# Kernel optimization log

Hardware: AMD Instinct MI355X
Metric: run time of the kernel (lower is better)

The kernel has to match this reference:

```python
import jax, jax.numpy as jnp
import numpy as np

N = 50000      # nodes
E = 800000     # edges
SEQ, SS = 96, 32
D = 128        # node feat dim = seqdim + ssdim
HE = 32        # edge hidden dim
HEADS = 4
DEPTH = 8
EPS = 1e-5
SLOPE = 0.01   # torch default leaky_relu slope (used in DGL EGATConv and LayerBlock)


def setup_inputs() -> dict:
    key = jax.random.key(0)
    ks = jax.random.split(key, 24)
    rn = lambda k, s: jax.random.normal(k, s, jnp.float32) * 0.1
    return {
        'sequence': jax.random.randint(ks[0], (N,), 0, 21),
        'secondary': jax.random.randint(ks[1], (N,), 0, 3),
        'edge_p': jax.random.uniform(ks[2], (E,), jnp.float32),
        'src': jax.random.randint(ks[3], (E,), 0, N),
        'dst': jax.random.randint(ks[4], (E,), 0, N),
        'Wseq': rn(ks[5], (21, SEQ)),
        'Wsec': rn(ks[6], (3, SS)),
        'W0_node': rn(ks[7], (D, D)), 'b0_node': jnp.zeros((D,), jnp.float32),
        'W0_ni': rn(ks[8], (D, HE)), 'W0_fij': rn(ks[9], (1, HE)),
        'W0_nj': rn(ks[10], (D, HE)), 'attn0': rn(ks[11], (1, HE)),
        'ebias0': jnp.zeros((HE,), jnp.float32),
        'Wn': rn(ks[12], (DEPTH, D, D)), 'bn': jnp.zeros((DEPTH, D), jnp.float32),
        'Wni': rn(ks[13], (DEPTH, D, HE)), 'Wfij': rn(ks[14], (DEPTH, HE, HE)),
        'Wnj': rn(ks[15], (DEPTH, D, HE)), 'attnB': rn(ks[16], (DEPTH, HEADS, HE // HEADS)),
        'ebiasB': jnp.zeros((DEPTH, HE), jnp.float32),
        'gn': jnp.ones((DEPTH, D), jnp.float32), 'betan': jnp.zeros((DEPTH, D), jnp.float32),
        'ge': jnp.ones((DEPTH, HE), jnp.float32), 'betae': jnp.zeros((DEPTH, HE), jnp.float32),
        'Wfc': rn(ks[17], (D, 1)), 'bfc': jnp.zeros((1,), jnp.float32),
    }


def _edge_softmax(logits, dst):
    # softmax over incoming edges of each destination node; logits: (E, H)
    m = jax.ops.segment_max(logits, dst, num_segments=N)
    m = jnp.where(jnp.isfinite(m), m, 0.0)
    z = jnp.exp(logits - m[dst])
    s = jax.ops.segment_sum(z, dst, num_segments=N)
    return z / s[dst]


def _egat(h, e, src, dst, Wnode, bnode, Wni_, Wfij_, Wnj_, attn, ebias, heads):
    # DGL EGATConv: h (N, Din), e (E, De) -> h_out (N, H, on), f_out (E, H, oe)
    oe = Wni_.shape[1] // heads
    on = Wnode.shape[1] // heads
    f = h[src] @ Wni_ + e @ Wfij_ + h[dst] @ Wnj_ + ebias          # (E, H*oe)
    f = jax.nn.leaky_relu(f, SLOPE).reshape(E, heads, oe)
    logits = jnp.einsum('ehd,hd->eh', f, attn)                      # (E, H)
    a = _edge_softmax(logits, dst)                                  # (E, H)
    hp = (h @ Wnode + bnode).reshape(N, heads, on)
    h_out = jax.ops.segment_sum(hp[src] * a[..., None], dst, num_segments=N)
    return h_out, f


def _batchnorm(x, gamma, beta):
    mu = x.mean(0)
    var = x.var(0)  # biased, as torch BN training mode
    return (x - mu) * jax.lax.rsqrt(var + EPS) * gamma + beta


def reference(sequence, secondary, edge_p, src, dst, Wseq, Wsec,
              W0_node, b0_node, W0_ni, W0_fij, W0_nj, attn0, ebias0,
              Wn, bn, Wni, Wfij, Wnj, attnB, ebiasB,
              gn, betan, ge, betae, Wfc, bfc):
    h = jnp.concatenate([Wseq[sequence], Wsec[secondary]], axis=1)   # (N, D)
    e = edge_p[:, None]                                              # (E, 1)
    h, f = _egat(h, e, src, dst, W0_node, b0_node, W0_ni, W0_fij, W0_nj, attn0, ebias0, 1)
    h = h.reshape(N, D)
    e = f.reshape(E, HE)

    def block(carry, p):
        hh, ee = carry
        Wn_, bn_, Wni_, Wfij_, Wnj_, attn_, eb_, gn_, btn_, ge_, bte_ = p
        h2, f2 = _egat(hh, ee, src, dst, Wn_, bn_, Wni_, Wfij_, Wnj_, attn_, eb_, HEADS)
        h2 = jax.nn.leaky_relu(_batchnorm(h2.reshape(N, D), gn_, btn_), SLOPE)
        e2 = jax.nn.leaky_relu(_batchnorm(f2.reshape(E, HE), ge_, bte_), SLOPE)
        return (h2, e2), None

    (h, e), _ = jax.lax.scan(block, (h, e),
                             (Wn, bn, Wni, Wfij, Wnj, attnB, ebiasB, gn, betan, ge, betae))
    return h @ Wfc + bfc                                             # (N, 1)
```

## Files before the change

### kernel.cpp

```cpp
#include <hip/hip_runtime.h>

#define NN 50000
#define NE 800000
#define D 128
#define HE 32
#define HEADS 4
#define DEPTH 8
#define EPSV 1e-5f
#define SLOPE 0.01f
#define CHUNK 196
#define SBH 512
#define SBE 1024

__device__ __forceinline__ float lrelu(float x) { return x > 0.f ? x : SLOPE * x; }

__device__ __forceinline__ float bf2f(unsigned short u) {
    union { float f; unsigned i; } c;
    c.i = ((unsigned)u) << 16;
    return c.f;
}
__device__ __forceinline__ unsigned short f2bf(float f) {
    union { float f; unsigned i; } c;
    c.f = f;
    unsigned r = c.i + 0x7FFFu + ((c.i >> 16) & 1u);
    return (unsigned short)(r >> 16);
}
__device__ __forceinline__ unsigned pack2(float a, float b) {
    return (unsigned)f2bf(a) | ((unsigned)f2bf(b) << 16);
}
__device__ __forceinline__ void unpk2(unsigned u, float& a, float& b) {
    union { float f; unsigned i; } c;
    c.i = u << 16; a = c.f;
    c.i = u & 0xFFFF0000u; b = c.f;
}

__global__ void k_init_h(const int* __restrict__ seq, const int* __restrict__ sec,
                         const float* __restrict__ Wseq, const float* __restrict__ Wsec,
                         float* __restrict__ h) {
    int n = blockIdx.x;
    int d = threadIdx.x;
    float v = (d < 96) ? Wseq[seq[n] * 96 + d] : Wsec[sec[n] * 32 + (d - 96)];
    h[(size_t)n * D + d] = v;
}

__global__ void k_count(const int* __restrict__ dst, int* __restrict__ cnt) {
    int e = blockIdx.x * blockDim.x + threadIdx.x;
    if (e < NE) atomicAdd(&cnt[dst[e]], 1);
}

__global__ void k_bsum(const int* __restrict__ cnt, int* __restrict__ bsum) {
    __shared__ int sh[256];
    int b = blockIdx.x, tid = threadIdx.x;
    int idx = b * CHUNK + tid;
    int v = (tid < CHUNK && idx < NN) ? cnt[idx] : 0;
    sh[tid] = v;
    __syncthreads();
    for (int st = 128; st >= 1; st >>= 1) {
        if (tid < st) sh[tid] += sh[tid + st];
        __syncthreads();
    }
    if (tid == 0) bsum[b] = sh[0];
}

__global__ void k_bscan(const int* __restrict__ bsum, int* __restrict__ bscan,
                        int* __restrict__ indptr) {
    __shared__ int sh[256];
    int tid = threadIdx.x;
    int v = bsum[tid];
    sh[tid] = v;
    __syncthreads();
    for (int st = 1; st < 256; st <<= 1) {
        int t = (tid >= st) ? sh[tid - st] : 0;
        __syncthreads();
        sh[tid] += t;
        __syncthreads();
    }
    bscan[tid] = sh[tid] - v;
    if (tid == 255) indptr[NN] = sh[255];
}

__global__ void k_bwrite(const int* __restrict__ cnt, const int* __restrict__ bscan,
                         int* __restrict__ indptr) {
    __shared__ int sh[256];
    int b = blockIdx.x, tid = threadIdx.x;
    int idx = b * CHUNK + tid;
    int v = (tid < CHUNK && idx < NN) ? cnt[idx] : 0;
    sh[tid] = v;
    __syncthreads();
    for (int st = 1; st < 256; st <<= 1) {
        int t = (tid >= st) ? sh[tid - st] : 0;
        __syncthreads();
        sh[tid] += t;
        __syncthreads();
    }
    if (tid < CHUNK && idx < NN) indptr[idx] = bscan[b] + sh[tid] - v;
}

__global__ void k_scatter(const int* __restrict__ dst, const int* __restrict__ indptr,
                          int* __restrict__ cursor, int* __restrict__ esort) {
    int e = blockIdx.x * blockDim.x + threadIdx.x;
    if (e >= NE) return;
    int dn = dst[e];
    int pos = atomicAdd(&cursor[dn], 1);
    esort[indptr[dn] + pos] = e;
}

__global__ void k_sortseg(const int* __restrict__ indptr, int* __restrict__ esort) {
    int n = blockIdx.x * blockDim.x + threadIdx.x;
    if (n >= NN) return;
    int b = indptr[n], e = indptr[n + 1];
    for (int i = b + 1; i < e; i++) {
        int v = esort[i];
        int j = i - 1;
        while (j >= b && esort[j] > v) {
            esort[j + 1] = esort[j];
            j--;
        }
        esort[j + 1] = v;
    }
}

__global__ void k_permute(const int* __restrict__ esort, const int* __restrict__ src,
                          const int* __restrict__ dst, const float* __restrict__ edge_p,
                          int* __restrict__ src_s, int* __restrict__ dst_s,
                          float* __restrict__ ep_s) {
    int i = blockIdx.x * blockDim.x + threadIdx.x;
    if (i >= NE) return;
    int e = esort[i];
    src_s[i] = src[e];
    dst_s[i] = dst[e];
    ep_s[i] = edge_p[e];
}

template <int APPLY_BN>
__global__ __launch_bounds__(256) void k_node(
    const float* __restrict__ hin, const float* __restrict__ scsh,
    const float* __restrict__ Wn_, const float* __restrict__ bn_,
    const float* __restrict__ Wni_, const float* __restrict__ Wnj_,
    unsigned short* __restrict__ hp, float* __restrict__ ni, float* __restrict__ nj) {
    __shared__ float hs[64][132];
    __shared__ float wb[2][8][192];
    int tid = threadIdx.x;
    int n0 = blockIdx.x * 64;

    float4 wreg[2];
    int wf0 = tid, wf1 = tid + 256;
    auto wload = [&](int s) {
#pragma unroll
        for (int u = 0; u < 2; u++) {
            int f = (u == 0) ? wf0 : wf1;
            if (f < 384) {
                int rr = f / 48, c = (f % 48) * 4;
                int dd = s * 8 + rr;
                const float* sp;
                if (c < 128) sp = Wn_ + (size_t)dd * 128 + c;
                else if (c < 160) sp = Wni_ + (size_t)dd * 32 + (c - 128);
                else sp = Wnj_ + (size_t)dd * 32 + (c - 160);
                wreg[u] = *(const float4*)sp;
            }
        }
    };
    auto wstore = [&](int buf) {
#pragma unroll
        for (int u = 0; u < 2; u++) {
            int f = (u == 0) ? wf0 : wf1;
            if (f < 384) {
                int rr = f / 48, c = (f % 48) * 4;
                *(float4*)&wb[buf][rr][c] = wreg[u];
            }
        }
    };

    wload(0);
#pragma unroll
    for (int k = 0; k < 8; k++) {
        int f = tid + k * 256;
        int r = f >> 5, c4 = f & 31;
        int row = n0 + r;
        if (row >= NN) row = NN - 1;
        float4 v = *(const float4*)(hin + (size_t)row * D + c4 * 4);
        if (APPLY_BN) {
            float4 sc = *(const float4*)(scsh + c4 * 4);
            float4 sh = *(const float4*)(scsh + 128 + c4 * 4);
            v.x = lrelu(v.x * sc.x + sh.x);
            v.y = lrelu(v.y * sc.y + sh.y);
            v.z = lrelu(v.z * sc.z + sh.z);
            v.w = lrelu(v.w * sc.w + sh.w);
        }
        *(float4*)(&hs[r][c4 * 4]) = v;
    }
    wstore(0);
    __syncthreads();

    int rg = tid >> 4;
    int cg = tid & 15;
    int pcol = 128 + (cg & 7) * 4 + ((cg < 8) ? 0 : 32);
    float4 bA = *(const float4*)(bn_ + cg * 4);
    float4 bB = *(const float4*)(bn_ + 64 + cg * 4);
    float4 accA[4], accB[4], accC[4];
#pragma unroll
    for (int r = 0; r < 4; r++) {
        accA[r] = bA;
        accB[r] = bB;
        accC[r] = make_float4(0.f, 0.f, 0.f, 0.f);
    }

#define FMA4(acc_, hv_, w_)                                     \
    (acc_).x += (hv_) * (w_).x; (acc_).y += (hv_) * (w_).y;     \
    (acc_).z += (hv_) * (w_).z; (acc_).w += (hv_) * (w_).w;

    for (int s = 0; s < 16; s++) {
        int cur = s & 1;
        if (s < 15) wload(s + 1);
#pragma unroll
        for (int dd = 0; dd < 8; dd++) {
            int d = s * 8 + dd;
            float h0 = hs[rg * 4 + 0][d];
            float h1 = hs[rg * 4 + 1][d];
            float h2 = hs[rg * 4 + 2][d];
            float h3 = hs[rg * 4 + 3][d];
            float4 wv0 = *(const float4*)&wb[cur][dd][cg * 4];
            float4 wv1 = *(const float4*)&wb[cur][dd][64 + cg * 4];
            float4 wv2 = *(const float4*)&wb[cur][dd][pcol];
            FMA4(accA[0], h0, wv0) FMA4(accA[1], h1, wv0)
            FMA4(accA[2], h2, wv0) FMA4(accA[3], h3, wv0)
            FMA4(accB[0], h0, wv1) FMA4(accB[1], h1, wv1)
            FMA4(accB[2], h2, wv1) FMA4(accB[3], h3, wv1)
            FMA4(accC[0], h0, wv2) FMA4(accC[1], h1, wv2)
            FMA4(accC[2], h2, wv2) FMA4(accC[3], h3, wv2)
        }
        __syncthreads();
        if (s < 15) {
            wstore((s + 1) & 1);
            __syncthreads();
        }
    }

    float* projOut = (cg < 8) ? ni : nj;
    int pc = (cg & 7) * 4;
#pragma unroll
    for (int r = 0; r < 4; r++) {
        int row = n0 + rg * 4 + r;
        if (row < NN) {
            ushort4 pa = make_ushort4(f2bf(accA[r].x), f2bf(accA[r].y), f2bf(accA[r].z),
                                      f2bf(accA[r].w));
            ushort4 pb = make_ushort4(f2bf(accB[r].x), f2bf(accB[r].y), f2bf(accB[r].z),
                                      f2bf(accB[r].w));
            *(ushort4*)(hp + (size_t)row * D + cg * 4) = pa;
            *(ushort4*)(hp + (size_t)row * D + 64 + cg * 4) = pb;
            *(float4*)(projOut + (size_t)row * HE + pc) = accC[r];
        }
    }
}

__global__ __launch_bounds__(256) void k_edge0(
    const float* __restrict__ ep_s, const int* __restrict__ src_s,
    const int* __restrict__ dst_s, const float* __restrict__ ni,
    const float* __restrict__ nj, const float* __restrict__ Wfij,
    const float* __restrict__ attn, const float* __restrict__ ebias,
    unsigned short* __restrict__ fout, float* __restrict__ logits) {
    __shared__ float sw[HE], sa[HE], se[HE];
    int tid = threadIdx.x;
    if (tid < HE) {
        sw[tid] = Wfij[tid];
        sa[tid] = attn[tid];
        se[tid] = ebias[tid];
    }
    __syncthreads();
    int i = blockIdx.x * blockDim.x + tid;
    if (i >= NE) return;
    int sn = src_s[i], dn = dst_s[i];
    float p = ep_s[i];
    const float4* niv = (const float4*)(ni + (size_t)sn * HE);
    const float4* njv = (const float4*)(nj + (size_t)dn * HE);
    float acc[HE];
#pragma unroll
    for (int j = 0; j < 8; j++) {
        float4 a = niv[j];
        float4 b = njv[j];
        acc[4 * j + 0] = se[4 * j + 0] + p * sw[4 * j + 0] + a.x + b.x;
        acc[4 * j + 1] = se[4 * j + 1] + p * sw[4 * j + 1] + a.y + b.y;
        acc[4 * j + 2] = se[4 * j + 2] + p * sw[4 * j + 2] + a.z + b.z;
        acc[4 * j + 3] = se[4 * j + 3] + p * sw[4 * j + 3] + a.w + b.w;
    }
    float lg = 0.f;
#pragma unroll
    for (int k = 0; k < HE; k++) {
        acc[k] = lrelu(acc[k]);
        lg += acc[k] * sa[k];
    }
    uint4* fo = (uint4*)(fout + (size_t)i * HE);
#pragma unroll
    for (int j = 0; j < 4; j++) {
        uint4 v;
        v.x = pack2(acc[8 * j + 0], acc[8 * j + 1]);
        v.y = pack2(acc[8 * j + 2], acc[8 * j + 3]);
        v.z = pack2(acc[8 * j + 4], acc[8 * j + 5]);
        v.w = pack2(acc[8 * j + 6], acc[8 * j + 7]);
        fo[j] = v;
    }
    logits[i] = lg;
}

template <int FIRST, int LAST>
__global__ __launch_bounds__(256) void k_edgeB(
    const unsigned short* __restrict__ e_in, const int* __restrict__ src_s,
    const int* __restrict__ dst_s, const float* __restrict__ ni,
    const float* __restrict__ nj, const float* __restrict__ Wfij,
    const float* __restrict__ attn, const float* __restrict__ ebias,
    const float* __restrict__ scsh,
    unsigned short* __restrict__ fout, float* __restrict__ logits) {
    int i = blockIdx.x * blockDim.x + threadIdx.x;
    if (i >= NE) return;
    int sn = src_s[i], dn = dst_s[i];
    const float4* niv = (const float4*)(ni + (size_t)sn * HE);
    const float4* njv = (const float4*)(nj + (size_t)dn * HE);
    float acc[HE];
#pragma unroll
    for (int j = 0; j < 8; j++) {
        float4 a = niv[j];
        float4 b = njv[j];
        acc[4 * j + 0] = ebias[4 * j + 0] + a.x + b.x;
        acc[4 * j + 1] = ebias[4 * j + 1] + a.y + b.y;
        acc[4 * j + 2] = ebias[4 * j + 2] + a.z + b.z;
        acc[4 * j + 3] = ebias[4 * j + 3] + a.w + b.w;
    }
    const uint4* ein4 = (const uint4*)(e_in + (size_t)i * HE);
#pragma unroll
    for (int j = 0; j < 4; j++) {
        uint4 ev = ein4[j];
        float ec[8];
        unpk2(ev.x, ec[0], ec[1]);
        unpk2(ev.y, ec[2], ec[3]);
        unpk2(ev.z, ec[4], ec[5]);
        unpk2(ev.w, ec[6], ec[7]);
#pragma unroll
        for (int c = 0; c < 8; c++) {
            int de = 8 * j + c;
            float x = ec[c];
            if (!FIRST) x = lrelu(x * scsh[256 + de] + scsh[288 + de]);
            const float* wr = Wfij + (size_t)de * HE;
#pragma unroll
            for (int k = 0; k < HE; k++) acc[k] += x * wr[k];
        }
    }
#pragma unroll
    for (int k = 0; k < HE; k++) acc[k] = lrelu(acc[k]);
    if (!LAST) {
        uint4* fo = (uint4*)(fout + (size_t)i * HE);
#pragma unroll
        for (int j = 0; j < 4; j++) {
            uint4 v;
            v.x = pack2(acc[8 * j + 0], acc[8 * j + 1]);
            v.y = pack2(acc[8 * j + 2], acc[8 * j + 3]);
            v.z = pack2(acc[8 * j + 4], acc[8 * j + 5]);
            v.w = pack2(acc[8 * j + 6], acc[8 * j + 7]);
            fo[j] = v;
        }
    }
#pragma unroll
    for (int hh = 0; hh < HEADS; hh++) {
        float s = 0.f;
#pragma unroll
        for (int j = 0; j < 8; j++) s += acc[hh * 8 + j] * attn[hh * 8 + j];
        logits[(size_t)hh * NE + i] = s;
    }
}

template <int H>
__global__ void k_smstat(const int* __restrict__ indptr, const float* __restrict__ logits,
                         float2* __restrict__ minv) {
    long t = (long)blockIdx.x * blockDim.x + threadIdx.x;
    if (t >= (long)NN * H) return;
    int n = (int)(t % NN);
    int hh = (int)(t / NN);
    const float* lp = logits + (size_t)hh * NE;
    int b = indptr[n], e = indptr[n + 1];
    if (b == e) {
        minv[(size_t)hh * NN + n] = make_float2(0.f, 0.f);
        return;
    }
    float m = -1e30f;
    for (int i = b; i < e; i++) m = fmaxf(m, lp[i]);
    float s = 0.f;
    for (int i = b; i < e; i++) s += __expf(lp[i] - m);
    minv[(size_t)hh * NN + n] = make_float2(m, 1.f / s);
}

template <int H>
__global__ __launch_bounds__(256) void k_aggregate(const int* __restrict__ indptr,
                                                   const int* __restrict__ src_s,
                                                   const float* __restrict__ logits,
                                                   const float2* __restrict__ minv,
                                                   const unsigned short* __restrict__ hp,
                                                   float* __restrict__ hacc) {
    int n = blockIdx.x * 4 + (threadIdx.x >> 6);
    if (n >= NN) return;
    int lane = threadIdx.x & 63;
    int c2 = lane * 2;
    int b = indptr[n], e = indptr[n + 1];
    int hh = (H == 1) ? 0 : (c2 >> 5);
    const float* lp = logits + (size_t)hh * NE;
    float2 mi = minv[(size_t)hh * NN + n];
    float acc0 = 0.f, acc1 = 0.f;
#pragma unroll 8
    for (int i = b; i < e; i++) {
        float w = __expf(lp[i] - mi.x) * mi.y;
        unsigned u = *(const unsigned*)(hp + (size_t)src_s[i] * D + c2);
        float x0, x1;
        unpk2(u, x0, x1);
        acc0 += w * x0;
        acc1 += w * x1;
    }
    *(float2*)(hacc + (size_t)n * D + c2) = make_float2(acc0, acc1);
}

__global__ __launch_bounds__(256) void k_bnstats(const float* __restrict__ xh,
                                                 const unsigned short* __restrict__ xe,
                                                 float* __restrict__ partialH,
                                                 float* __restrict__ partialE) {
    int tid = threadIdx.x;
    if (blockIdx.x < SBH) {
        __shared__ float4 shs[256], shq[256];
        int c4 = (tid & 31) * 4;
        int r0 = tid >> 5;
        float4 s = make_float4(0.f, 0.f, 0.f, 0.f);
        float4 q = make_float4(0.f, 0.f, 0.f, 0.f);
        for (long r = (long)blockIdx.x * 8 + r0; r < NN; r += (long)SBH * 8) {
            float4 v = *(const float4*)(xh + r * D + c4);
            s.x += v.x; s.y += v.y; s.z += v.z; s.w += v.w;
            q.x += v.x * v.x; q.y += v.y * v.y; q.z += v.z * v.z; q.w += v.w * v.w;
        }
        shs[tid] = s;
        shq[tid] = q;
        __syncthreads();
        for (int st = 128; st >= 32; st >>= 1) {
            if (tid < st) {
                float4 a = shs[tid], b = shs[tid + st];
                a.x += b.x; a.y += b.y; a.z += b.z; a.w += b.w;
                shs[tid] = a;
                float4 c = shq[tid], d = shq[tid + st];
                c.x += d.x; c.y += d.y; c.z += d.z; c.w += d.w;
                shq[tid] = c;
            }
            __syncthreads();
        }
        if (tid < 32) {
            *(float4*)&partialH[(size_t)blockIdx.x * 256 + 4 * tid] = shs[tid];
            *(float4*)&partialH[(size_t)blockIdx.x * 256 + 128 + 4 * tid] = shq[tid];
        }
    } else {
        __shared__ float shs0[256], shs1[256], shq0[256], shq1[256];
        int blk = blockIdx.x - SBH;
        int d = tid & 15;
        int r0 = tid >> 4;
        float s0 = 0.f, s1 = 0.f, q0 = 0.f, q1 = 0.f;
        for (long r = (long)blk * 16 + r0; r < NE; r += (long)SBE * 16) {
            unsigned u = *(const unsigned*)(xe + r * HE + 2 * d);
            float a, b;
            unpk2(u, a, b);
            s0 += a; s1 += b;
            q0 += a * a; q1 += b * b;
        }
        shs0[tid] = s0; shs1[tid] = s1;
        shq0[tid] = q0; shq1[tid] = q1;
        __syncthreads();
        for (int st = 128; st >= 16; st >>= 1) {
            if (tid < st) {
                shs0[tid] += shs0[tid + st];
                shs1[tid] += shs1[tid + st];
                shq0[tid] += shq0[tid + st];
                shq1[tid] += shq1[tid + st];
            }
            __syncthreads();
        }
        if (tid < 16) {
            partialE[(size_t)blk * 64 + 2 * tid] = shs0[tid];
            partialE[(size_t)blk * 64 + 2 * tid + 1] = shs1[tid];
            partialE[(size_t)blk * 64 + 32 + 2 * tid] = shq0[tid];
            partialE[(size_t)blk * 64 + 32 + 2 * tid + 1] = shq1[tid];
        }
    }
}

__global__ __launch_bounds__(256) void k_bnprep(const float* __restrict__ partialH,
                                                const float* __restrict__ gH,
                                                const float* __restrict__ bH,
                                                const float* __restrict__ partialE,
                                                const float* __restrict__ gE,
                                                const float* __restrict__ bE,
                                                float* __restrict__ scsh, int doE) {
    __shared__ float sh[512];
    int f = blockIdx.x;
    int tid = threadIdx.x;
    if (f < 128) {
        float s = 0.f, s2 = 0.f;
        for (int b = tid; b < SBH; b += 256) {
            s += partialH[(size_t)b * 256 + f];
            s2 += partialH[(size_t)b * 256 + 128 + f];
        }
        sh[tid] = s;
        sh[256 + tid] = s2;
        __syncthreads();
        for (int st = 128; st >= 1; st >>= 1) {
            if (tid < st) {
                sh[tid] += sh[tid + st];
                sh[256 + tid] += sh[256 + tid + st];
            }
            __syncthreads();
        }
        if (tid == 0) {
            float mu = sh[0] * (1.f / NN);
            float var = sh[256] * (1.f / NN) - mu * mu;
            float sc = rsqrtf(var + EPSV) * gH[f];
            scsh[f] = sc;
            scsh[128 + f] = bH[f] - mu * sc;
        }
    } else {
        if (!doE) return;
        int k = f - 128;
        float s = 0.f, s2 = 0.f;
        for (int b = tid; b < SBE; b += 256) {
            s += partialE[(size_t)b * 64 + k];
            s2 += partialE[(size_t)b * 64 + 32 + k];
        }
        sh[tid] = s;
        sh[256 + tid] = s2;
        __syncthreads();
        for (int st = 128; st >= 1; st >>= 1) {
            if (tid < st) {
                sh[tid] += sh[tid + st];
                sh[256 + tid] += sh[256 + tid + st];
            }
            __syncthreads();
        }
        if (tid == 0) {
            float mu = sh[0] * (1.f / NE);
            float var = sh[256] * (1.f / NE) - mu * mu;
            float sc = rsqrtf(var + EPSV) * gE[k];
            scsh[256 + k] = sc;
            scsh[288 + k] = bE[k] - mu * sc;
        }
    }
}

__global__ void k_out(const float* __restrict__ h, const float* __restrict__ scsh,
                      const float* __restrict__ Wfc, const float* __restrict__ bfc,
                      float* __restrict__ out) {
    int n = blockIdx.x * blockDim.x + threadIdx.x;
    if (n >= NN) return;
    const float* hr = h + (size_t)n * D;
    float s = bfc[0];
    for (int d = 0; d < D; d++) {
        float v = lrelu(hr[d] * scsh[d] + scsh[128 + d]);
        s += v * Wfc[d];
    }
    out[n] = s;
}

extern "C" void kernel_launch(void* const* d_in, const int* in_sizes, int n_in,
                              void* d_out, int out_size, void* d_ws, size_t ws_size,
                              hipStream_t stream) {
    const int* seq = (const int*)d_in[0];
    const int* sec = (const int*)d_in[1];
    const float* edge_p = (const float*)d_in[2];
    const int* src = (const int*)d_in[3];
    const int* dst = (const int*)d_in[4];
    const float* Wseq = (const float*)d_in[5];
    const float* Wsec = (const float*)d_in[6];
    const float* W0_node = (const float*)d_in[7];
    const float* b0_node = (const float*)d_in[8];
    const float* W0_ni = (const float*)d_in[9];
    const float* W0_fij = (const float*)d_in[10];
    const float* W0_nj = (const float*)d_in[11];
    const float* attn0 = (const float*)d_in[12];
    const float* ebias0 = (const float*)d_in[13];
    const float* Wn = (const float*)d_in[14];
    const float* bn = (const float*)d_in[15];
    const float* Wni = (const float*)d_in[16];
    const float* Wfij = (const float*)d_in[17];
    const float* Wnj = (const float*)d_in[18];
    const float* attnB = (const float*)d_in[19];
    const float* ebiasB = (const float*)d_in[20];
    const float* gn = (const float*)d_in[21];
    const float* betan = (const float*)d_in[22];
    const float* ge = (const float*)d_in[23];
    const float* betae = (const float*)d_in[24];
    const float* Wfc = (const float*)d_in[25];
    const float* bfc = (const float*)d_in[26];

    char* p = (char*)d_ws;
    auto alloc = [&](size_t bytes) -> char* {
        char* r = p;
        p += (bytes + 255) & ~(size_t)255;
        return r;
    };
    float* hA = (float*)alloc((size_t)NN * D * 4);
    float* hB = (float*)alloc((size_t)NN * D * 4);
    unsigned short* hp = (unsigned short*)alloc((size_t)NN * D * 2);
    unsigned short* ebuf = (unsigned short*)alloc((size_t)NE * HE * 2);
    float* logits = (float*)alloc((size_t)NE * HEADS * 4);
    float2* minv = (float2*)alloc((size_t)HEADS * NN * 8);
    float* ni = (float*)alloc((size_t)NN * HE * 4);
    float* nj = (float*)alloc((size_t)NN * HE * 4);
    int* esort = (int*)alloc((size_t)NE * 4);
    int* src_s = (int*)alloc((size_t)NE * 4);
    int* dst_s = (int*)alloc((size_t)NE * 4);
    float* ep_s = (float*)alloc((size_t)NE * 4);
    int* cnt = (int*)alloc((size_t)NN * 4);
    int* cursor = (int*)alloc((size_t)NN * 4);
    int* indptr = (int*)alloc((size_t)(NN + 1) * 4);
    int* bsum = (int*)alloc(256 * 4);
    int* bscan = (int*)alloc(256 * 4);
    float* partialH = (float*)alloc((size_t)SBH * 256 * 4);
    float* partialE = (float*)alloc((size_t)SBE * 64 * 4);
    float* scsh0 = (float*)alloc(320 * 4);
    float* scsh1 = (float*)alloc(320 * 4);

    const int EB = (NE + 255) / 256;
    const int NB64 = (NN + 63) / 64;

    hipMemsetAsync(cnt, 0, (size_t)NN * 4, stream);
    hipMemsetAsync(cursor, 0, (size_t)NN * 4, stream);
    k_init_h<<<NN, 128, 0, stream>>>(seq, sec, Wseq, Wsec, hB);
    k_count<<<EB, 256, 0, stream>>>(dst, cnt);
    k_bsum<<<256, 256, 0, stream>>>(cnt, bsum);
    k_bscan<<<1, 256, 0, stream>>>(bsum, bscan, indptr);
    k_bwrite<<<256, 256, 0, stream>>>(cnt, bscan, indptr);
    k_scatter<<<EB, 256, 0, stream>>>(dst, indptr, cursor, esort);
    k_sortseg<<<(NN + 255) / 256, 256, 0, stream>>>(indptr, esort);
    k_permute<<<EB, 256, 0, stream>>>(esort, src, dst, edge_p, src_s, dst_s, ep_s);

    k_node<0><<<NB64, 256, 0, stream>>>(hB, scsh0, W0_node, b0_node, W0_ni, W0_nj, hp, ni, nj);
    k_edge0<<<EB, 256, 0, stream>>>(ep_s, src_s, dst_s, ni, nj, W0_fij, attn0, ebias0, ebuf,
                                    logits);
    k_smstat<1><<<(NN + 255) / 256, 256, 0, stream>>>(indptr, logits, minv);
    k_aggregate<1><<<(NN + 3) / 4, 256, 0, stream>>>(indptr, src_s, logits, minv, hp, hA);

    for (int l = 0; l < DEPTH; l++) {
        const float* Wn_l = Wn + (size_t)l * D * D;
        const float* bn_l = bn + (size_t)l * D;
        const float* Wni_l = Wni + (size_t)l * D * HE;
        const float* Wfij_l = Wfij + (size_t)l * HE * HE;
        const float* Wnj_l = Wnj + (size_t)l * D * HE;
        const float* attn_l = attnB + (size_t)l * HE;
        const float* eb_l = ebiasB + (size_t)l * HE;
        float* scshPrev = (l & 1) ? scsh0 : scsh1;
        float* scshCur = (l & 1) ? scsh1 : scsh0;
        float* hIn = (l & 1) ? hB : hA;
        float* hOut = (l & 1) ? hA : hB;
        int doE = (l < DEPTH - 1) ? 1 : 0;

        if (l == 0)
            k_node<0><<<NB64, 256, 0, stream>>>(hIn, scshPrev, Wn_l, bn_l, Wni_l, Wnj_l, hp,
                                                ni, nj);
        else
            k_node<1><<<NB64, 256, 0, stream>>>(hIn, scshPrev, Wn_l, bn_l, Wni_l, Wnj_l, hp,
                                                ni, nj);

        if (l == 0)
            k_edgeB<1, 0><<<EB, 256, 0, stream>>>(ebuf, src_s, dst_s, ni, nj, Wfij_l, attn_l,
                                                  eb_l, scshPrev, ebuf, logits);
        else if (l == DEPTH - 1)
            k_edgeB<0, 1><<<EB, 256, 0, stream>>>(ebuf, src_s, dst_s, ni, nj, Wfij_l, attn_l,
                                                  eb_l, scshPrev, ebuf, logits);
        else
            k_edgeB<0, 0><<<EB, 256, 0, stream>>>(ebuf, src_s, dst_s, ni, nj, Wfij_l, attn_l,
                                                  eb_l, scshPrev, ebuf, logits);
        k_smstat<HEADS><<<(NN * HEADS + 255) / 256, 256, 0, stream>>>(indptr, logits, minv);
        k_aggregate<HEADS><<<(NN + 3) / 4, 256, 0, stream>>>(indptr, src_s, logits, minv, hp,
                                                             hOut);

        k_bnstats<<<SBH + (doE ? SBE : 0), 256, 0, stream>>>(hOut, ebuf, partialH, partialE);
        k_bnprep<<<160, 256, 0, stream>>>(partialH, gn + (size_t)l * D, betan + (size_t)l * D,
                                          partialE, ge + (size_t)l * HE, betae + (size_t)l * HE,
                                          scshCur, doE);
    }

    k_out<<<(NN + 255) / 256, 256, 0, stream>>>(hA, scsh1, Wfc, bfc, (float*)d_out);
}
```

Measured before the change: 2.058 ms.

## Fuse edge-softmax stats into aggregation and process two edges per thread

The separate softmax-statistics kernel is removed. Each wavefront now computes the per-destination max and sum cooperatively with shuffle reductions before aggregating, which drops a launch and the minv round trip and replaces serial per-thread segment scans with a strided parallel scan. The edge kernel now handles two edges per thread in two 16-column halves, reusing each Wfij load for both edges and cutting register pressure per pass. The cost is re-reading logits three times inside aggregation and half as many edge threads.

New measurement: 1.938 ms. 5.9% less time.

```diff
diff --git a/kernel.cpp b/kernel.cpp
--- a/kernel.cpp
+++ b/kernel.cpp
@@ -310,102 +310,139 @@
     const float* __restrict__ attn, const float* __restrict__ ebias,
     const float* __restrict__ scsh,
     unsigned short* __restrict__ fout, float* __restrict__ logits) {
-    int i = blockIdx.x * blockDim.x + threadIdx.x;
-    if (i >= NE) return;
-    int sn = src_s[i], dn = dst_s[i];
-    const float4* niv = (const float4*)(ni + (size_t)sn * HE);
-    const float4* njv = (const float4*)(nj + (size_t)dn * HE);
-    float acc[HE];
-#pragma unroll
-    for (int j = 0; j < 8; j++) {
-        float4 a = niv[j];
-        float4 b = njv[j];
-        acc[4 * j + 0] = ebias[4 * j + 0] + a.x + b.x;
-        acc[4 * j + 1] = ebias[4 * j + 1] + a.y + b.y;
-        acc[4 * j + 2] = ebias[4 * j + 2] + a.z + b.z;
-        acc[4 * j + 3] = ebias[4 * j + 3] + a.w + b.w;
-    }
-    const uint4* ein4 = (const uint4*)(e_in + (size_t)i * HE);
-#pragma unroll
-    for (int j = 0; j < 4; j++) {
-        uint4 ev = ein4[j];
-        float ec[8];
-        unpk2(ev.x, ec[0], ec[1]);
-        unpk2(ev.y, ec[2], ec[3]);
-        unpk2(ev.z, ec[4], ec[5]);
-        unpk2(ev.w, ec[6], ec[7]);
-#pragma unroll
-        for (int c = 0; c < 8; c++) {
-            int de = 8 * j + c;
-            float x = ec[c];
-            if (!FIRST) x = lrelu(x * scsh[256 + de] + scsh[288 + de]);
-            const float* wr = Wfij + (size_t)de * HE;
-#pragma unroll
-            for (int k = 0; k < HE; k++) acc[k] += x * wr[k];
-        }
-    }
-#pragma unroll
-    for (int k = 0; k < HE; k++) acc[k] = lrelu(acc[k]);
-    if (!LAST) {
-        uint4* fo = (uint4*)(fout + (size_t)i * HE);
+    int tid = threadIdx.x;
+    int i0 = blockIdx.x * 512 + tid;
+    if (i0 >= NE) return;
+    int i1 = i0 + 256;
+    bool v1 = i1 < NE;
+    int i1s = v1 ? i1 : i0;
+    int sn0 = src_s[i0], dn0 = dst_s[i0];
+    int sn1 = src_s[i1s], dn1 = dst_s[i1s];
+    const uint4* ein0 = (const uint4*)(e_in + (size_t)i0 * HE);
+    const uint4* ein1 = (const uint4*)(e_in + (size_t)i1s * HE);
+
+    for (int half = 0; half < 2; half++) {
+        int k0 = half * 16;
+        float acc0[16], acc1[16];
+        {
+            const float4* a0 = (const float4*)(ni + (size_t)sn0 * HE + k0);
+            const float4* b0 = (const float4*)(nj + (size_t)dn0 * HE + k0);
+            const float4* a1 = (const float4*)(ni + (size_t)sn1 * HE + k0);
+            const float4* b1 = (const float4*)(nj + (size_t)dn1 * HE + k0);
+            const float4* eb4 = (const float4*)(ebias + k0);
+#pragma unroll
+            for (int j4 = 0; j4 < 4; j4++) {
+                float4 va0 = a0[j4], vb0 = b0[j4];
+                float4 va1 = a1[j4], vb1 = b1[j4];
+                float4 eb = eb4[j4];
+                acc0[4 * j4 + 0] = eb.x + va0.x + vb0.x;
+                acc0[4 * j4 + 1] = eb.y + va0.y + vb0.y;
+                acc0[4 * j4 + 2] = eb.z + va0.z + vb0.z;
+                acc0[4 * j4 + 3] = eb.w + va0.w + vb0.w;
+                acc1[4 * j4 + 0] = eb.x + va1.x + vb1.x;
+                acc1[4 * j4 + 1] = eb.y + va1.y + vb1.y;
+                acc1[4 * j4 + 2] = eb.z + va1.z + vb1.z;
+                acc1[4 * j4 + 3] = eb.w + va1.w + vb1.w;
+            }
+        }
 #pragma unroll
         for (int j = 0; j < 4; j++) {
-            uint4 v;
-            v.x = pack2(acc[8 * j + 0], acc[8 * j + 1]);
-            v.y = pack2(acc[8 * j + 2], acc[8 * j + 3]);
-            v.z = pack2(acc[8 * j + 4], acc[8 * j + 5]);
-            v.w = pack2(acc[8 * j + 6], acc[8 * j + 7]);
-            fo[j] = v;
-        }
-    }
-#pragma unroll
-    for (int hh = 0; hh < HEADS; hh++) {
-        float s = 0.f;
-#pragma unroll
-        for (int j = 0; j < 8; j++) s += acc[hh * 8 + j] * attn[hh * 8 + j];
-        logits[(size_t)hh * NE + i] = s;
+            uint4 ev0 = ein0[j];
+            uint4 ev1 = ein1[j];
+            float ec0[8], ec1[8];
+            unpk2(ev0.x, ec0[0], ec0[1]); unpk2(ev0.y, ec0[2], ec0[3]);
+            unpk2(ev0.z, ec0[4], ec0[5]); unpk2(ev0.w, ec0[6], ec0[7]);
+            unpk2(ev1.x, ec1[0], ec1[1]); unpk2(ev1.y, ec1[2], ec1[3]);
+            unpk2(ev1.z, ec1[4], ec1[5]); unpk2(ev1.w, ec1[6], ec1[7]);
+#pragma unroll
+            for (int c = 0; c < 8; c++) {
+                int de = 8 * j + c;
+                float x0 = ec0[c], x1 = ec1[c];
+                if (!FIRST) {
+                    float sc = scsh[256 + de], sh = scsh[288 + de];
+                    x0 = lrelu(x0 * sc + sh);
+                    x1 = lrelu(x1 * sc + sh);
+                }
+                const float4* wr = (const float4*)(Wfij + (size_t)de * HE + k0);
+#pragma unroll
+                for (int k4 = 0; k4 < 4; k4++) {
+                    float4 w = wr[k4];
+                    acc0[4 * k4 + 0] += x0 * w.x; acc1[4 * k4 + 0] += x1 * w.x;
+                    acc0[4 * k4 + 1] += x0 * w.y; acc1[4 * k4 + 1] += x1 * w.y;
+                    acc0[4 * k4 + 2] += x0 * w.z; acc1[4 * k4 + 2] += x1 * w.z;
+                    acc0[4 * k4 + 3] += x0 * w.w; acc1[4 * k4 + 3] += x1 * w.w;
+                }
+            }
+        }
+#pragma unroll
+        for (int k = 0; k < 16; k++) {
+            acc0[k] = lrelu(acc0[k]);
+            acc1[k] = lrelu(acc1[k]);
+        }
+        if (!LAST) {
+            uint4 v0a, v0b;
+            v0a.x = pack2(acc0[0], acc0[1]);  v0a.y = pack2(acc0[2], acc0[3]);
+            v0a.z = pack2(acc0[4], acc0[5]);  v0a.w = pack2(acc0[6], acc0[7]);
+            v0b.x = pack2(acc0[8], acc0[9]);  v0b.y = pack2(acc0[10], acc0[11]);
+            v0b.z = pack2(acc0[12], acc0[13]); v0b.w = pack2(acc0[14], acc0[15]);
+            *(uint4*)(fout + (size_t)i0 * HE + k0) = v0a;
+            *(uint4*)(fout + (size_t)i0 * HE + k0 + 8) = v0b;
+            if (v1) {
+                uint4 v1a, v1b;
+                v1a.x = pack2(acc1[0], acc1[1]);  v1a.y = pack2(acc1[2], acc1[3]);
+                v1a.z = pack2(acc1[4], acc1[5]);  v1a.w = pack2(acc1[6], acc1[7]);
+                v1b.x = pack2(acc1[8], acc1[9]);  v1b.y = pack2(acc1[10], acc1[11]);
+                v1b.z = pack2(acc1[12], acc1[13]); v1b.w = pack2(acc1[14], acc1[15]);
+                *(uint4*)(fout + (size_t)i1 * HE + k0) = v1a;
+                *(uint4*)(fout + (size_t)i1 * HE + k0 + 8) = v1b;
+            }
+        }
+#pragma unroll
+        for (int hh2 = 0; hh2 < 2; hh2++) {
+            int hh = half * 2 + hh2;
+            float s0 = 0.f, s1 = 0.f;
+#pragma unroll
+            for (int j = 0; j < 8; j++) {
+                float av = attn[hh * 8 + j];
+                s0 += acc0[hh2 * 8 + j] * av;
+                s1 += acc1[hh2 * 8 + j] * av;
+            }
+            logits[(size_t)hh * NE + i0] = s0;
+            if (v1) logits[(size_t)hh * NE + i1] = s1;
+        }
     }
 }
 
 template <int H>
-__global__ void k_smstat(const int* __restrict__ indptr, const float* __restrict__ logits,
-                         float2* __restrict__ minv) {
-    long t = (long)blockIdx.x * blockDim.x + threadIdx.x;
-    if (t >= (long)NN * H) return;
-    int n = (int)(t % NN);
-    int hh = (int)(t / NN);
-    const float* lp = logits + (size_t)hh * NE;
-    int b = indptr[n], e = indptr[n + 1];
-    if (b == e) {
-        minv[(size_t)hh * NN + n] = make_float2(0.f, 0.f);
-        return;
-    }
-    float m = -1e30f;
-    for (int i = b; i < e; i++) m = fmaxf(m, lp[i]);
-    float s = 0.f;
-    for (int i = b; i < e; i++) s += __expf(lp[i] - m);
-    minv[(size_t)hh * NN + n] = make_float2(m, 1.f / s);
-}
-
-template <int H>
-__global__ __launch_bounds__(256) void k_aggregate(const int* __restrict__ indptr,
-                                                   const int* __restrict__ src_s,
-                                                   const float* __restrict__ logits,
-                                                   const float2* __restrict__ minv,
-                                                   const unsigned short* __restrict__ hp,
-                                                   float* __restrict__ hacc) {
+__global__ __launch_bounds__(256) void k_aggsm(const int* __restrict__ indptr,
+                                               const int* __restrict__ src_s,
+                                               const float* __restrict__ logits,
+                                               const unsigned short* __restrict__ hp,
+                                               float* __restrict__ hacc) {
     int n = blockIdx.x * 4 + (threadIdx.x >> 6);
     if (n >= NN) return;
     int lane = threadIdx.x & 63;
     int c2 = lane * 2;
     int b = indptr[n], e = indptr[n + 1];
-    int hh = (H == 1) ? 0 : (c2 >> 5);
+    int hh = (H == 1) ? 0 : (lane >> 4);
     const float* lp = logits + (size_t)hh * NE;
-    float2 mi = minv[(size_t)hh * NN + n];
+    const int stride = (H == 1) ? 64 : 16;
+    int sub = (H == 1) ? lane : (lane & 15);
+    float m = -1e30f;
+    for (int i = b + sub; i < e; i += stride) m = fmaxf(m, lp[i]);
+#pragma unroll
+    for (int w = 32; w >= 1; w >>= 1)
+        if (w < stride) m = fmaxf(m, __shfl_xor(m, w));
+    float s = 0.f;
+    for (int i = b + sub; i < e; i += stride) s += __expf(lp[i] - m);
+#pragma unroll
+    for (int w = 32; w >= 1; w >>= 1)
+        if (w < stride) s += __shfl_xor(s, w);
+    float inv = (e > b) ? 1.f / s : 0.f;
     float acc0 = 0.f, acc1 = 0.f;
-#pragma unroll 8
+#pragma unroll 4
     for (int i = b; i < e; i++) {
-        float w = __expf(lp[i] - mi.x) * mi.y;
+        float w = __expf(lp[i] - m) * inv;
         unsigned u = *(const unsigned*)(hp + (size_t)src_s[i] * D + c2);
         float x0, x1;
         unpk2(u, x0, x1);
@@ -600,7 +637,6 @@
     unsigned short* hp = (unsigned short*)alloc((size_t)NN * D * 2);
     unsigned short* ebuf = (unsigned short*)alloc((size_t)NE * HE * 2);
     float* logits = (float*)alloc((size_t)NE * HEADS * 4);
-    float2* minv = (float2*)alloc((size_t)HEADS * NN * 8);
     float* ni = (float*)alloc((size_t)NN * HE * 4);
     float* nj = (float*)alloc((size_t)NN * HE * 4);
     int* esort = (int*)alloc((size_t)NE * 4);
@@ -618,6 +654,7 @@
     float* scsh1 = (float*)alloc(320 * 4);
 
     const int EB = (NE + 255) / 256;
+    const int EB2 = (NE + 511) / 512;
     const int NB64 = (NN + 63) / 64;
 
     hipMemsetAsync(cnt, 0, (size_t)NN * 4, stream);
@@ -634,8 +671,7 @@
     k_node<0><<<NB64, 256, 0, stream>>>(hB, scsh0, W0_node, b0_node, W0_ni, W0_nj, hp, ni, nj);
     k_edge0<<<EB, 256, 0, stream>>>(ep_s, src_s, dst_s, ni, nj, W0_fij, attn0, ebias0, ebuf,
                                     logits);
-    k_smstat<1><<<(NN + 255) / 256, 256, 0, stream>>>(indptr, logits, minv);
-    k_aggregate<1><<<(NN + 3) / 4, 256, 0, stream>>>(indptr, src_s, logits, minv, hp, hA);
+    k_aggsm<1><<<(NN + 3) / 4, 256, 0, stream>>>(indptr, src_s, logits, hp, hA);
 
     for (int l = 0; l < DEPTH; l++) {
         const float* Wn_l = Wn + (size_t)l * D * D;
@@ -659,17 +695,15 @@
                                                 ni, nj);
 
         if (l == 0)
-            k_edgeB<1, 0><<<EB, 256, 0, stream>>>(ebuf, src_s, dst_s, ni, nj, Wfij_l, attn_l,
-                                                  eb_l, scshPrev, ebuf, logits);
+            k_edgeB<1, 0><<<EB2, 256, 0, stream>>>(ebuf, src_s, dst_s, ni, nj, Wfij_l, attn_l,
+                                                   eb_l, scshPrev, ebuf, logits);
         else if (l == DEPTH - 1)
-            k_edgeB<0, 1><<<EB, 256, 0, stream>>>(ebuf, src_s, dst_s, ni, nj, Wfij_l, attn_l,
-                                                  eb_l, scshPrev, ebuf, logits);
+            k_edgeB<0, 1><<<EB2, 256, 0, stream>>>(ebuf, src_s, dst_s, ni, nj, Wfij_l, attn_l,
+                                                   eb_l, scshPrev, ebuf, logits);
         else
-            k_edgeB<0, 0><<<EB, 256, 0, stream>>>(ebuf, src_s, dst_s, ni, nj, Wfij_l, attn_l,
-                                                  eb_l, scshPrev, ebuf, logits);
-        k_smstat<HEADS><<<(NN * HEADS + 255) / 256, 256, 0, stream>>>(indptr, logits, minv);
-        k_aggregate<HEADS><<<(NN + 3) / 4, 256, 0, stream>>>(indptr, src_s, logits, minv, hp,
-                                                             hOut);
+            k_edgeB<0, 0><<<EB2, 256, 0, stream>>>(ebuf, src_s, dst_s, ni, nj, Wfij_l, attn_l,
+                                                   eb_l, scshPrev, ebuf, logits);
+        k_aggsm<HEADS><<<(NN + 3) / 4, 256, 0, stream>>>(indptr, src_s, logits, hp, hOut);
 
         k_bnstats<<<SBH + (doE ? SBE : 0), 256, 0, stream>>>(hOut, ebuf, partialH, partialE);
         k_bnprep<<<160, 256, 0, stream>>>(partialH, gn + (size_t)l * D, betan + (size_t)l * D,
```
